# Performance work log

Hardware: AMD Instinct MI355X
Metric: run time of the kernel (lower is better)

The kernel has to match this reference:

```python
import jax, jax.numpy as jnp
import numpy as np

D = 128
SCALE = 1.0 / np.sqrt(D).astype(np.float32)


def setup_inputs() -> dict:
    key = jax.random.key(0)
    kq, kk, kv = jax.random.split(key, 3)
    B, L = 16, 2048
    q = jax.random.normal(kq, (B, L, D), dtype=jnp.float32)
    k = jax.random.normal(kk, (B, L, D), dtype=jnp.float32)
    v = jax.random.normal(kv, (B, L, D), dtype=jnp.float32)
    return {"q": q, "k": k, "v": v}


def reference(q, k, v):
    # attention[b, i, j] = sum_d q[b,i,d] * k[b,j,d], scaled
    scores = jnp.einsum('bqd,bkd->bqk', q, k) * SCALE
    attention = jax.nn.softmax(scores, axis=2)
    # dropout p=0.0 -> identity
    context = jnp.einsum('bqk,bkd->bqd', attention, v)
    return (context, attention)
```

## Files before the change

kernel.cpp:

```cpp
#include <hip/hip_runtime.h>
#include <hip/hip_bf16.h>

#define NB 16
#define NL 2048
#define ND 128
#define QSCALE 0.08838834764831845f

using short8 = __attribute__((ext_vector_type(8))) short;
using f32x4  = __attribute__((ext_vector_type(4))) float;

__device__ __forceinline__ unsigned short bfr(float f) {
  unsigned u = __float_as_uint(f);
  unsigned r = u + 0x7FFFu + ((u >> 16) & 1u);
  return (unsigned short)(r >> 16);
}
__device__ __forceinline__ float bf2f(unsigned short h) {
  return __uint_as_float(((unsigned)h) << 16);
}

#define WS_KB 0
#define WS_VT 8388608
#define WS_LINV 16777216
#define WS_NEED 16908288

__global__ __launch_bounds__(256)
void prep_k(const float* __restrict__ kg, unsigned short* __restrict__ Kb) {
  size_t base = ((size_t)blockIdx.x * 256 + threadIdx.x) * 4;
  float4 x = *(const float4*)(kg + base);
  ushort4 o;
  o.x = bfr(x.x); o.y = bfr(x.y); o.z = bfr(x.z); o.w = bfr(x.w);
  *(ushort4*)(Kb + base) = o;
}

__global__ __launch_bounds__(256)
void prep_vt(const float* __restrict__ vg, unsigned short* __restrict__ Vt) {
  __shared__ float T[32][129];
  const int b = blockIdx.y, j0 = blockIdx.x * 32, tid = threadIdx.x;
  const float* vb = vg + ((size_t)b * NL + j0) * ND;
#pragma unroll
  for (int r = 0; r < 4; ++r) {
    int f4 = tid + r * 256;
    int j  = f4 >> 5;
    int c4 = f4 & 31;
    float4 x = *(const float4*)(vb + (size_t)j * ND + c4 * 4);
    T[j][c4 * 4 + 0] = x.x; T[j][c4 * 4 + 1] = x.y;
    T[j][c4 * 4 + 2] = x.z; T[j][c4 * 4 + 3] = x.w;
  }
  __syncthreads();
  const int d = tid >> 1, h = tid & 1;
  unsigned short* orow = Vt + ((size_t)b * ND + d) * NL + j0 + h * 16;
#pragma unroll
  for (int g = 0; g < 4; ++g) {
    ushort4 o;
    o.x = bfr(T[h * 16 + g * 4 + 0][d]);
    o.y = bfr(T[h * 16 + g * 4 + 1][d]);
    o.z = bfr(T[h * 16 + g * 4 + 2][d]);
    o.w = bfr(T[h * 16 + g * 4 + 3][d]);
    *(ushort4*)(orow + g * 4) = o;
  }
}

__device__ __forceinline__ void load_q_frags(const float* qrow, int quad,
                                             short8* qh, short8* ql) {
#pragma unroll
  for (int kk = 0; kk < 4; ++kk) {
    const float* p = qrow + kk * 32 + quad * 8;
    float4 x = *(const float4*)(p);
    float4 y = *(const float4*)(p + 4);
    float e[8] = {x.x, x.y, x.z, x.w, y.x, y.y, y.z, y.w};
    short8 th, tl;
#pragma unroll
    for (int t = 0; t < 8; ++t) {
      float qs = e[t] * QSCALE;
      unsigned short h = bfr(qs);
      th[t] = (short)h;
      tl[t] = (short)bfr(qs - bf2f(h));
    }
    qh[kk] = th;
    ql[kk] = tl;
  }
}

__global__ __launch_bounds__(256, 2)
void attn_ctx(const float* __restrict__ q, const unsigned short* __restrict__ Kb,
              const unsigned short* __restrict__ Vt,
              float* __restrict__ ctx, float* __restrict__ linv_ws) {
  __shared__ unsigned short Ks[128][132];
  __shared__ unsigned short Vs[128][132];
  __shared__ unsigned short Ps[4][16][36];

  const int b    = blockIdx.y;
  const int i0   = blockIdx.x * 64;
  const int tid  = threadIdx.x;
  const int wave = tid >> 6;
  const int lane = tid & 63;
  const int quad = lane >> 4;
  const int l16  = lane & 15;

  const float* qrow = q + ((size_t)b * NL + i0 + wave * 16 + l16) * ND;
  short8 qh[4], ql[4];
  load_q_frags(qrow, quad, qh, ql);

  f32x4 oacc[8];
#pragma unroll
  for (int i = 0; i < 8; ++i) oacc[i] = (f32x4){0.f, 0.f, 0.f, 0.f};
  float lsum[4] = {0.f, 0.f, 0.f, 0.f};

  const unsigned short* kbb = Kb + (size_t)b * NL * ND;
  const unsigned short* vtb = Vt + (size_t)b * ND * NL;

  for (int j0 = 0; j0 < NL; j0 += 128) {
    __syncthreads();
#pragma unroll
    for (int r = 0; r < 8; ++r) {
      int c = tid + r * 256;
      int row = c >> 4, c8 = c & 15;
      *(short8*)&Ks[row][c8 * 8] =
          *(const short8*)(kbb + (size_t)(j0 + row) * ND + c8 * 8);
    }
#pragma unroll
    for (int r = 0; r < 8; ++r) {
      int c = tid + r * 256;
      int d = c >> 4, c8 = c & 15;
      *(short8*)&Vs[d][c8 * 8] =
          *(const short8*)(vtb + (size_t)d * NL + j0 + c8 * 8);
    }
    __syncthreads();

#pragma unroll
    for (int ks = 0; ks < 4; ++ks) {
      f32x4 a0 = {0.f, 0.f, 0.f, 0.f}, a1 = {0.f, 0.f, 0.f, 0.f};
#pragma unroll
      for (int kk = 0; kk < 4; ++kk) {
        short8 k0 = *(const short8*)&Ks[ks * 32 + l16][kk * 32 + quad * 8];
        short8 k1 = *(const short8*)&Ks[ks * 32 + 16 + l16][kk * 32 + quad * 8];
        a0 = __builtin_amdgcn_mfma_f32_16x16x32_bf16(qh[kk], k0, a0, 0, 0, 0);
        a0 = __builtin_amdgcn_mfma_f32_16x16x32_bf16(ql[kk], k0, a0, 0, 0, 0);
        a1 = __builtin_amdgcn_mfma_f32_16x16x32_bf16(qh[kk], k1, a1, 0, 0, 0);
        a1 = __builtin_amdgcn_mfma_f32_16x16x32_bf16(ql[kk], k1, a1, 0, 0, 0);
      }
#pragma unroll
      for (int r = 0; r < 4; ++r) {
        float e0 = __expf(a0[r]);
        float e1 = __expf(a1[r]);
        lsum[r] += e0 + e1;
        Ps[wave][quad * 4 + r][l16]      = bfr(e0);
        Ps[wave][quad * 4 + r][l16 + 16] = bfr(e1);
      }
      short8 pa = *(const short8*)&Ps[wave][l16][quad * 8];
#pragma unroll
      for (int dt = 0; dt < 8; ++dt) {
        short8 vf = *(const short8*)&Vs[dt * 16 + l16][ks * 32 + quad * 8];
        oacc[dt] = __builtin_amdgcn_mfma_f32_16x16x32_bf16(pa, vf, oacc[dt], 0, 0, 0);
      }
    }
  }

#pragma unroll
  for (int r = 0; r < 4; ++r) {
    float s = lsum[r];
    s += __shfl_xor(s, 1, 16);
    s += __shfl_xor(s, 2, 16);
    s += __shfl_xor(s, 4, 16);
    s += __shfl_xor(s, 8, 16);
    float li = 1.0f / s;
    if (l16 == 0)
      linv_ws[(size_t)b * NL + i0 + wave * 16 + quad * 4 + r] = li;
    float* crow = ctx + ((size_t)b * NL + i0 + wave * 16 + quad * 4 + r) * ND;
#pragma unroll
    for (int dt = 0; dt < 8; ++dt)
      crow[dt * 16 + l16] = oacc[dt][r] * li;
  }
}

__global__ __launch_bounds__(256, 4)
void attn_probs(const float* __restrict__ q, const unsigned short* __restrict__ Kb,
                const float* __restrict__ linv_ws, float* __restrict__ attn) {
  __shared__ unsigned short Ks[128][136];

  const int b    = blockIdx.z;
  const int i0   = blockIdx.y * 64;
  const int j0   = blockIdx.x * 128;
  const int tid  = threadIdx.x;
  const int wave = tid >> 6;
  const int lane = tid & 63;
  const int quad = lane >> 4;
  const int l16  = lane & 15;
  const int row0 = i0 + wave * 16;

  const float* qrow = q + ((size_t)b * NL + row0 + l16) * ND;
  short8 qh[4], ql[4];
  load_q_frags(qrow, quad, qh, ql);

  float li[4];
#pragma unroll
  for (int r = 0; r < 4; ++r)
    li[r] = linv_ws[(size_t)b * NL + row0 + quad * 4 + r];

  const unsigned short* kbb = Kb + (size_t)b * NL * ND;
#pragma unroll
  for (int r = 0; r < 8; ++r) {
    int c = tid + r * 256;
    int row = c >> 4, c8 = c & 15;
    *(short8*)&Ks[row][c8 * 8] =
        *(const short8*)(kbb + (size_t)(j0 + row) * ND + c8 * 8);
  }
  __syncthreads();

#pragma unroll
  for (int jg = 0; jg < 8; ++jg) {
    f32x4 a = {0.f, 0.f, 0.f, 0.f};
#pragma unroll
    for (int kk = 0; kk < 4; ++kk) {
      short8 kf = *(const short8*)&Ks[jg * 16 + l16][kk * 32 + quad * 8];
      a = __builtin_amdgcn_mfma_f32_16x16x32_bf16(qh[kk], kf, a, 0, 0, 0);
      a = __builtin_amdgcn_mfma_f32_16x16x32_bf16(ql[kk], kf, a, 0, 0, 0);
    }
    float* arow = attn + ((size_t)b * NL + row0 + quad * 4) * NL + j0 + jg * 16;
#pragma unroll
    for (int r = 0; r < 4; ++r)
      arow[(size_t)r * NL + l16] = __expf(a[r]) * li[r];
  }
}

__global__ __launch_bounds__(256, 2)
void attn_fused(const float* __restrict__ q, const float* __restrict__ kg,
                const float* __restrict__ vg, float* __restrict__ out) {
  float* ctx  = out;
  float* attn = out + (size_t)NB * NL * ND;
  const int b    = blockIdx.y;
  const int i0   = blockIdx.x * 64;
  const int tid  = threadIdx.x;
  const int wave = tid >> 6;
  const int lane = tid & 63;
  const int quad = lane >> 4;
  const int l16  = lane & 15;

  __shared__ short Ksf[32][136];
  __shared__ short Vtf[128][40];
  __shared__ short Ps2[4][16][40];

  const float* qrow = q + ((size_t)b * NL + i0 + wave * 16 + l16) * ND;
  short8 qh[4], ql[4];
  load_q_frags(qrow, quad, qh, ql);

  f32x4 oacc[8];
#pragma unroll
  for (int i = 0; i < 8; ++i) oacc[i] = (f32x4){0.f, 0.f, 0.f, 0.f};
  float lsum[4] = {0.f, 0.f, 0.f, 0.f};

  const float* kb = kg + (size_t)b * NL * ND;
  const float* vb = vg + (size_t)b * NL * ND;

  for (int j0 = 0; j0 < NL; j0 += 32) {
    __syncthreads();
#pragma unroll
    for (int rr = 0; rr < 4; ++rr) {
      int idx = tid + rr * 256;
      int row = idx >> 5;
      int c4  = idx & 31;
      float4 kv = *(const float4*)(kb + (size_t)(j0 + row) * ND + c4 * 4);
      ushort4 ks;
      ks.x = bfr(kv.x); ks.y = bfr(kv.y); ks.z = bfr(kv.z); ks.w = bfr(kv.w);
      *(ushort4*)&Ksf[row][c4 * 4] = ks;
      float4 vv = *(const float4*)(vb + (size_t)(j0 + row) * ND + c4 * 4);
      Vtf[c4 * 4 + 0][row] = (short)bfr(vv.x);
      Vtf[c4 * 4 + 1][row] = (short)bfr(vv.y);
      Vtf[c4 * 4 + 2][row] = (short)bfr(vv.z);
      Vtf[c4 * 4 + 3][row] = (short)bfr(vv.w);
    }
    __syncthreads();

    f32x4 a0 = {0.f, 0.f, 0.f, 0.f}, a1 = {0.f, 0.f, 0.f, 0.f};
#pragma unroll
    for (int kk = 0; kk < 4; ++kk) {
      short8 k0 = *(const short8*)&Ksf[l16][kk * 32 + quad * 8];
      short8 k1 = *(const short8*)&Ksf[l16 + 16][kk * 32 + quad * 8];
      a0 = __builtin_amdgcn_mfma_f32_16x16x32_bf16(qh[kk], k0, a0, 0, 0, 0);
      a0 = __builtin_amdgcn_mfma_f32_16x16x32_bf16(ql[kk], k0, a0, 0, 0, 0);
      a1 = __builtin_amdgcn_mfma_f32_16x16x32_bf16(qh[kk], k1, a1, 0, 0, 0);
      a1 = __builtin_amdgcn_mfma_f32_16x16x32_bf16(ql[kk], k1, a1, 0, 0, 0);
    }
#pragma unroll
    for (int r = 0; r < 4; ++r) {
      float e0 = __expf(a0[r]);
      float e1 = __expf(a1[r]);
      lsum[r] += e0 + e1;
      Ps2[wave][quad * 4 + r][l16]      = (short)bfr(e0);
      Ps2[wave][quad * 4 + r][l16 + 16] = (short)bfr(e1);
    }
    __syncthreads();
    short8 pa = *(const short8*)&Ps2[wave][l16][quad * 8];
#pragma unroll
    for (int dt = 0; dt < 8; ++dt) {
      short8 vf = *(const short8*)&Vtf[dt * 16 + l16][quad * 8];
      oacc[dt] = __builtin_amdgcn_mfma_f32_16x16x32_bf16(pa, vf, oacc[dt], 0, 0, 0);
    }
  }

  float linv[4];
#pragma unroll
  for (int r = 0; r < 4; ++r) {
    float s = lsum[r];
    s += __shfl_xor(s, 1, 16);
    s += __shfl_xor(s, 2, 16);
    s += __shfl_xor(s, 4, 16);
    s += __shfl_xor(s, 8, 16);
    linv[r] = 1.0f / s;
  }
#pragma unroll
  for (int r = 0; r < 4; ++r) {
    float* crow = ctx + ((size_t)b * NL + i0 + wave * 16 + quad * 4 + r) * ND;
#pragma unroll
    for (int dt = 0; dt < 8; ++dt)
      crow[dt * 16 + l16] = oacc[dt][r] * linv[r];
  }

  for (int j0 = 0; j0 < NL; j0 += 32) {
    __syncthreads();
#pragma unroll
    for (int rr = 0; rr < 4; ++rr) {
      int idx = tid + rr * 256;
      int row = idx >> 5;
      int c4  = idx & 31;
      float4 kv = *(const float4*)(kb + (size_t)(j0 + row) * ND + c4 * 4);
      ushort4 ks;
      ks.x = bfr(kv.x); ks.y = bfr(kv.y); ks.z = bfr(kv.z); ks.w = bfr(kv.w);
      *(ushort4*)&Ksf[row][c4 * 4] = ks;
    }
    __syncthreads();
    f32x4 a0 = {0.f, 0.f, 0.f, 0.f}, a1 = {0.f, 0.f, 0.f, 0.f};
#pragma unroll
    for (int kk = 0; kk < 4; ++kk) {
      short8 k0 = *(const short8*)&Ksf[l16][kk * 32 + quad * 8];
      short8 k1 = *(const short8*)&Ksf[l16 + 16][kk * 32 + quad * 8];
      a0 = __builtin_amdgcn_mfma_f32_16x16x32_bf16(qh[kk], k0, a0, 0, 0, 0);
      a0 = __builtin_amdgcn_mfma_f32_16x16x32_bf16(ql[kk], k0, a0, 0, 0, 0);
      a1 = __builtin_amdgcn_mfma_f32_16x16x32_bf16(qh[kk], k1, a1, 0, 0, 0);
      a1 = __builtin_amdgcn_mfma_f32_16x16x32_bf16(ql[kk], k1, a1, 0, 0, 0);
    }
    float* arow = attn + ((size_t)b * NL + i0 + wave * 16 + quad * 4) * NL + j0;
#pragma unroll
    for (int r = 0; r < 4; ++r) {
      arow[(size_t)r * NL + l16]      = __expf(a0[r]) * linv[r];
      arow[(size_t)r * NL + l16 + 16] = __expf(a1[r]) * linv[r];
    }
  }
}

extern "C" void kernel_launch(void* const* d_in, const int* in_sizes, int n_in,
                              void* d_out, int out_size, void* d_ws, size_t ws_size,
                              hipStream_t stream) {
  const float* q = (const float*)d_in[0];
  const float* k = (const float*)d_in[1];
  const float* v = (const float*)d_in[2];
  float* out = (float*)d_out;

  if (ws_size >= (size_t)WS_NEED) {
    unsigned short* Kb = (unsigned short*)((char*)d_ws + WS_KB);
    unsigned short* Vt = (unsigned short*)((char*)d_ws + WS_VT);
    float* linv        = (float*)((char*)d_ws + WS_LINV);
    float* ctx  = out;
    float* attn = out + (size_t)NB * NL * ND;

    prep_k<<<dim3(4096), dim3(256), 0, stream>>>(k, Kb);
    prep_vt<<<dim3(64, 16), dim3(256), 0, stream>>>(v, Vt);
    attn_ctx<<<dim3(32, 16), dim3(256), 0, stream>>>(q, Kb, Vt, ctx, linv);
    attn_probs<<<dim3(16, 32, 16), dim3(256), 0, stream>>>(q, Kb, linv, attn);
  } else {
    dim3 grid(NL / 64, NB);
    attn_fused<<<grid, dim3(256), 0, stream>>>(q, k, v, out);
  }
}
```

Before: 484.1 us.

## Use async global-to-LDS loads with XOR swizzle, exp2 softmax, and transposed MFMA outputs

Replaces the register-staged K/V tile copies into padded shared memory with direct global_load_lds transfers into an XOR-swizzled layout. Q is prescaled by log2(e) so the hardware exp2 can be used in place of expf. Swapping the MFMA operand order transposes the score tile, so each lane holds one query row. That allows packed bf16 writes of P, a per-row sum with two shuffles, and 16-byte vector stores of the attention matrix. The risk is the more complex async load path and its reliance on correct swizzle and LDS addressing.

```diff
diff --git a/kernel.cpp b/kernel.cpp
--- a/kernel.cpp
+++ b/kernel.cpp
@@ -5,9 +5,14 @@
 #define NL 2048
 #define ND 128
 #define QSCALE 0.08838834764831845f
+#define QSCALE2 (0.08838834764831845f * 1.4426950408889634f)
 
 using short8 = __attribute__((ext_vector_type(8))) short;
 using f32x4  = __attribute__((ext_vector_type(4))) float;
+
+__device__ __forceinline__ float hw_exp2(float x) {
+  return __builtin_amdgcn_exp2f(x);
+}
 
 __device__ __forceinline__ unsigned short bfr(float f) {
   unsigned u = __float_as_uint(f);
@@ -16,6 +21,19 @@
 }
 __device__ __forceinline__ float bf2f(unsigned short h) {
   return __uint_as_float(((unsigned)h) << 16);
+}
+__device__ __forceinline__ unsigned pk(float a, float b) {
+  return (unsigned)bfr(a) | ((unsigned)bfr(b) << 16);
+}
+
+typedef const __attribute__((address_space(1))) unsigned int* gas1_t;
+typedef __attribute__((address_space(3))) unsigned int* las3_t;
+__device__ __forceinline__ void async_lds16(const unsigned short* g, unsigned short* l) {
+  __builtin_amdgcn_global_load_lds((gas1_t)g, (las3_t)l, 16, 0, 0);
+}
+
+__device__ __forceinline__ short8 swz_frag(const unsigned short* base, int row, int chunk) {
+  return *(const short8*)(base + row * 128 + (((chunk ^ (row & 7)) << 3)));
 }
 
 #define WS_KB 0
@@ -61,7 +79,7 @@
 }
 
 __device__ __forceinline__ void load_q_frags(const float* qrow, int quad,
-                                             short8* qh, short8* ql) {
+                                             short8* qh, short8* ql, float scale) {
 #pragma unroll
   for (int kk = 0; kk < 4; ++kk) {
     const float* p = qrow + kk * 32 + quad * 8;
@@ -71,7 +89,7 @@
     short8 th, tl;
 #pragma unroll
     for (int t = 0; t < 8; ++t) {
-      float qs = e[t] * QSCALE;
+      float qs = e[t] * scale;
       unsigned short h = bfr(qs);
       th[t] = (short)h;
       tl[t] = (short)bfr(qs - bf2f(h));
@@ -85,8 +103,8 @@
 void attn_ctx(const float* __restrict__ q, const unsigned short* __restrict__ Kb,
               const unsigned short* __restrict__ Vt,
               float* __restrict__ ctx, float* __restrict__ linv_ws) {
-  __shared__ unsigned short Ks[128][132];
-  __shared__ unsigned short Vs[128][132];
+  __shared__ unsigned short KsL[128 * 128];
+  __shared__ unsigned short VsL[128 * 128];
   __shared__ unsigned short Ps[4][16][36];
 
   const int b    = blockIdx.y;
@@ -99,12 +117,12 @@
 
   const float* qrow = q + ((size_t)b * NL + i0 + wave * 16 + l16) * ND;
   short8 qh[4], ql[4];
-  load_q_frags(qrow, quad, qh, ql);
+  load_q_frags(qrow, quad, qh, ql, QSCALE2);
 
   f32x4 oacc[8];
 #pragma unroll
   for (int i = 0; i < 8; ++i) oacc[i] = (f32x4){0.f, 0.f, 0.f, 0.f};
-  float lsum[4] = {0.f, 0.f, 0.f, 0.f};
+  float lsum = 0.f;
 
   const unsigned short* kbb = Kb + (size_t)b * NL * ND;
   const unsigned short* vtb = Vt + (size_t)b * ND * NL;
@@ -113,17 +131,17 @@
     __syncthreads();
 #pragma unroll
     for (int r = 0; r < 8; ++r) {
-      int c = tid + r * 256;
-      int row = c >> 4, c8 = c & 15;
-      *(short8*)&Ks[row][c8 * 8] =
-          *(const short8*)(kbb + (size_t)(j0 + row) * ND + c8 * 8);
+      int row = wave * 4 + r * 16 + (lane >> 4);
+      int c   = lane & 15;
+      async_lds16(kbb + (size_t)(j0 + row) * ND + ((c ^ (row & 7)) << 3),
+                  KsL + (wave * 64 + r * 256) * 8);
     }
 #pragma unroll
     for (int r = 0; r < 8; ++r) {
-      int c = tid + r * 256;
-      int d = c >> 4, c8 = c & 15;
-      *(short8*)&Vs[d][c8 * 8] =
-          *(const short8*)(vtb + (size_t)d * NL + j0 + c8 * 8);
+      int d = wave * 4 + r * 16 + (lane >> 4);
+      int c = lane & 15;
+      async_lds16(vtb + (size_t)d * NL + j0 + ((c ^ (d & 7)) << 3),
+                  VsL + (wave * 64 + r * 256) * 8);
     }
     __syncthreads();
 
@@ -132,51 +150,54 @@
       f32x4 a0 = {0.f, 0.f, 0.f, 0.f}, a1 = {0.f, 0.f, 0.f, 0.f};
 #pragma unroll
       for (int kk = 0; kk < 4; ++kk) {
-        short8 k0 = *(const short8*)&Ks[ks * 32 + l16][kk * 32 + quad * 8];
-        short8 k1 = *(const short8*)&Ks[ks * 32 + 16 + l16][kk * 32 + quad * 8];
-        a0 = __builtin_amdgcn_mfma_f32_16x16x32_bf16(qh[kk], k0, a0, 0, 0, 0);
-        a0 = __builtin_amdgcn_mfma_f32_16x16x32_bf16(ql[kk], k0, a0, 0, 0, 0);
-        a1 = __builtin_amdgcn_mfma_f32_16x16x32_bf16(qh[kk], k1, a1, 0, 0, 0);
-        a1 = __builtin_amdgcn_mfma_f32_16x16x32_bf16(ql[kk], k1, a1, 0, 0, 0);
+        short8 k0 = swz_frag(KsL, ks * 32 + l16, kk * 4 + quad);
+        short8 k1 = swz_frag(KsL, ks * 32 + 16 + l16, kk * 4 + quad);
+        a0 = __builtin_amdgcn_mfma_f32_16x16x32_bf16(k0, qh[kk], a0, 0, 0, 0);
+        a0 = __builtin_amdgcn_mfma_f32_16x16x32_bf16(k0, ql[kk], a0, 0, 0, 0);
+        a1 = __builtin_amdgcn_mfma_f32_16x16x32_bf16(k1, qh[kk], a1, 0, 0, 0);
+        a1 = __builtin_amdgcn_mfma_f32_16x16x32_bf16(k1, ql[kk], a1, 0, 0, 0);
       }
+      float e0[4], e1[4];
 #pragma unroll
       for (int r = 0; r < 4; ++r) {
-        float e0 = __expf(a0[r]);
-        float e1 = __expf(a1[r]);
-        lsum[r] += e0 + e1;
-        Ps[wave][quad * 4 + r][l16]      = bfr(e0);
-        Ps[wave][quad * 4 + r][l16 + 16] = bfr(e1);
+        e0[r] = hw_exp2(a0[r]);
+        e1[r] = hw_exp2(a1[r]);
+        lsum += e0[r] + e1[r];
       }
+      uint2 w0, w1;
+      w0.x = pk(e0[0], e0[1]); w0.y = pk(e0[2], e0[3]);
+      w1.x = pk(e1[0], e1[1]); w1.y = pk(e1[2], e1[3]);
+      *(uint2*)&Ps[wave][l16][quad * 4]      = w0;
+      *(uint2*)&Ps[wave][l16][16 + quad * 4] = w1;
       short8 pa = *(const short8*)&Ps[wave][l16][quad * 8];
 #pragma unroll
       for (int dt = 0; dt < 8; ++dt) {
-        short8 vf = *(const short8*)&Vs[dt * 16 + l16][ks * 32 + quad * 8];
+        short8 vf = swz_frag(VsL, dt * 16 + l16, ks * 4 + quad);
         oacc[dt] = __builtin_amdgcn_mfma_f32_16x16x32_bf16(pa, vf, oacc[dt], 0, 0, 0);
       }
     }
   }
 
+  lsum += __shfl_xor(lsum, 16);
+  lsum += __shfl_xor(lsum, 32);
+  float sinv = 1.0f / lsum;
+  if (lane < 16)
+    linv_ws[(size_t)b * NL + i0 + wave * 16 + lane] = sinv;
+
 #pragma unroll
   for (int r = 0; r < 4; ++r) {
-    float s = lsum[r];
-    s += __shfl_xor(s, 1, 16);
-    s += __shfl_xor(s, 2, 16);
-    s += __shfl_xor(s, 4, 16);
-    s += __shfl_xor(s, 8, 16);
-    float li = 1.0f / s;
-    if (l16 == 0)
-      linv_ws[(size_t)b * NL + i0 + wave * 16 + quad * 4 + r] = li;
+    float lir = __shfl(sinv, quad * 4 + r, 16);
     float* crow = ctx + ((size_t)b * NL + i0 + wave * 16 + quad * 4 + r) * ND;
 #pragma unroll
     for (int dt = 0; dt < 8; ++dt)
-      crow[dt * 16 + l16] = oacc[dt][r] * li;
+      crow[dt * 16 + l16] = oacc[dt][r] * lir;
   }
 }
 
 __global__ __launch_bounds__(256, 4)
 void attn_probs(const float* __restrict__ q, const unsigned short* __restrict__ Kb,
                 const float* __restrict__ linv_ws, float* __restrict__ attn) {
-  __shared__ unsigned short Ks[128][136];
+  __shared__ unsigned short KsL[128 * 128];
 
   const int b    = blockIdx.z;
   const int i0   = blockIdx.y * 64;
@@ -188,23 +209,20 @@
   const int l16  = lane & 15;
   const int row0 = i0 + wave * 16;
 
+  const unsigned short* kbb = Kb + (size_t)b * NL * ND;
+#pragma unroll
+  for (int r = 0; r < 8; ++r) {
+    int row = wave * 4 + r * 16 + (lane >> 4);
+    int c   = lane & 15;
+    async_lds16(kbb + (size_t)(j0 + row) * ND + ((c ^ (row & 7)) << 3),
+                KsL + (wave * 64 + r * 256) * 8);
+  }
+
   const float* qrow = q + ((size_t)b * NL + row0 + l16) * ND;
   short8 qh[4], ql[4];
-  load_q_frags(qrow, quad, qh, ql);
-
-  float li[4];
-#pragma unroll
-  for (int r = 0; r < 4; ++r)
-    li[r] = linv_ws[(size_t)b * NL + row0 + quad * 4 + r];
-
-  const unsigned short* kbb = Kb + (size_t)b * NL * ND;
-#pragma unroll
-  for (int r = 0; r < 8; ++r) {
-    int c = tid + r * 256;
-    int row = c >> 4, c8 = c & 15;
-    *(short8*)&Ks[row][c8 * 8] =
-        *(const short8*)(kbb + (size_t)(j0 + row) * ND + c8 * 8);
-  }
+  load_q_frags(qrow, quad, qh, ql, QSCALE2);
+  float li = linv_ws[(size_t)b * NL + row0 + l16];
+
   __syncthreads();
 
 #pragma unroll
@@ -212,14 +230,14 @@
     f32x4 a = {0.f, 0.f, 0.f, 0.f};
 #pragma unroll
     for (int kk = 0; kk < 4; ++kk) {
-      short8 kf = *(const short8*)&Ks[jg * 16 + l16][kk * 32 + quad * 8];
-      a = __builtin_amdgcn_mfma_f32_16x16x32_bf16(qh[kk], kf, a, 0, 0, 0);
-      a = __builtin_amdgcn_mfma_f32_16x16x32_bf16(ql[kk], kf, a, 0, 0, 0);
-    }
-    float* arow = attn + ((size_t)b * NL + row0 + quad * 4) * NL + j0 + jg * 16;
-#pragma unroll
-    for (int r = 0; r < 4; ++r)
-      arow[(size_t)r * NL + l16] = __expf(a[r]) * li[r];
+      short8 kf = swz_frag(KsL, jg * 16 + l16, kk * 4 + quad);
+      a = __builtin_amdgcn_mfma_f32_16x16x32_bf16(kf, qh[kk], a, 0, 0, 0);
+      a = __builtin_amdgcn_mfma_f32_16x16x32_bf16(kf, ql[kk], a, 0, 0, 0);
+    }
+    f32x4 o;
+#pragma unroll
+    for (int r = 0; r < 4; ++r) o[r] = hw_exp2(a[r]) * li;
+    *(f32x4*)(attn + ((size_t)b * NL + row0 + l16) * NL + j0 + jg * 16 + quad * 4) = o;
   }
 }
 
@@ -242,7 +260,7 @@
 
   const float* qrow = q + ((size_t)b * NL + i0 + wave * 16 + l16) * ND;
   short8 qh[4], ql[4];
-  load_q_frags(qrow, quad, qh, ql);
+  load_q_frags(qrow, quad, qh, ql, QSCALE);
 
   f32x4 oacc[8];
 #pragma unroll
```

New measurement: 399.3 us. 1.21x faster.
